# Optimization experiments

Measured on AMD Instinct MI355X. Metric: run time of the kernel, lower is better.

The kernel has to match this reference:

```python
import jax, jax.numpy as jnp
import numpy as np

B, N, C_Q, H, C_HID = 1, 2048, 256, 8, 32


def setup_inputs() -> dict:
    key = jax.random.key(0)
    ks = jax.random.split(key, 8)
    s_in = 1.0 / np.sqrt(C_Q)
    s_hid = 1.0 / np.sqrt(H * C_HID)
    return {
        "q_x": jax.random.normal(ks[0], (B, N, C_Q), jnp.float32),
        "kv_x": jax.random.normal(ks[1], (B, N, C_Q), jnp.float32),
        "attn_bias": jax.random.normal(ks[2], (B, H, N, N), jnp.float32),
        "Wq": jax.random.normal(ks[3], (C_Q, H * C_HID), jnp.float32) * s_in,
        "Wk": jax.random.normal(ks[4], (C_Q, H * C_HID), jnp.float32) * s_in,
        "Wv": jax.random.normal(ks[5], (C_Q, H * C_HID), jnp.float32) * s_in,
        "Wg": jax.random.normal(ks[6], (C_Q, H * C_HID), jnp.float32) * s_in,
        "Wo": jax.random.normal(ks[7], (H * C_HID, C_Q), jnp.float32) * s_hid,
    }


def reference(q_x, kv_x, attn_bias, Wq, Wk, Wv, Wg, Wo):
    # QKV projections (no bias), split heads: [B, H, N, C_hid]
    def proj(x, W):
        y = x @ W  # [B, N, H*C_hid]
        return y.reshape(y.shape[:-1] + (H, C_HID)).swapaxes(-2, -3)

    scale = 1.0 / np.sqrt(C_HID)
    q = proj(q_x, Wq) * scale
    k = proj(kv_x, Wk)
    v = proj(kv_x, Wv)

    # scores + external additive bias, stable softmax
    scores = jnp.einsum("bhqc,bhkc->bhqk", q, k) + attn_bias
    a = jax.nn.softmax(scores, axis=-1)
    o = jnp.einsum("bhqk,bhkc->bhqc", a, v)  # [B, H, N, C_hid]

    o = o.swapaxes(-2, -3)  # [B, N, H, C_hid]
    # sigmoid gating from query input
    g = jax.nn.sigmoid(q_x @ Wg).reshape(o.shape)
    o = o * g
    o = o.reshape(o.shape[:-2] + (H * C_HID,))
    return o @ Wo  # [B, N, C_q]
```

## Files before the change

kernel.cpp:

```cpp
#include <hip/hip_runtime.h>
#include <hip/hip_bf16.h>
#include <stdint.h>

typedef __attribute__((ext_vector_type(8))) short short8;
typedef __attribute__((ext_vector_type(8))) __bf16 bf16x8;
typedef __attribute__((ext_vector_type(4))) float f32x4;
typedef __attribute__((ext_vector_type(4))) float float4v;
typedef __attribute__((ext_vector_type(4))) unsigned short us4;
typedef unsigned int u32;
typedef __attribute__((ext_vector_type(2))) u32 u32x2;
typedef __attribute__((address_space(3))) u32 lds_u32;
typedef const __attribute__((address_space(1))) u32 g_u32;

#define NSEQ 2048
#define L2E 1.44269504088896f

static __device__ __forceinline__ unsigned short f2bf(float x){
  union { float f; u32 u; } v; v.f = x;
  u32 r = v.u + 0x7fffu + ((v.u >> 16) & 1u);
  return (unsigned short)(r >> 16);
}
static __device__ __forceinline__ float bf2f(unsigned short s){
  union { float f; u32 u; } v; v.u = ((u32)s) << 16; return v.f;
}
static __device__ __forceinline__ u32 cvtpk(float lo, float hi){
  u32 r; asm("v_cvt_pk_bf16_f32 %0, %1, %2" : "=v"(r) : "v"(lo), "v"(hi)); return r;
}
static __device__ __forceinline__ void gload16(const void* g, void* l){
  __builtin_amdgcn_global_load_lds((g_u32*)g, (lds_u32*)l, 16, 0, 0);
}
static __device__ __forceinline__ f32x4 mfma16(bf16x8 a, bf16x8 b, f32x4 c){
  return __builtin_amdgcn_mfma_f32_16x16x32_bf16(a, b, c, 0, 0, 0);
}
static __device__ __forceinline__ bf16x8 ldfrag(const void* p){
  return *(const bf16x8*)p;
}
#define MEMFENCE() asm volatile("" ::: "memory")

__global__ __launch_bounds__(256) void cvt_kernel(const float* __restrict__ qx,
                           const float* __restrict__ kvx,
                           const float* __restrict__ Wq, const float* __restrict__ Wk,
                           const float* __restrict__ Wv, const float* __restrict__ Wg,
                           const float* __restrict__ Wo,
                           unsigned short* __restrict__ Xbq, unsigned short* __restrict__ Xbkv,
                           unsigned short* __restrict__ Wt4, unsigned short* __restrict__ Wot){
  __shared__ float T[64][65];
  int bid = blockIdx.x;
  if (bid < 512){
    int i4 = (bid*256 + threadIdx.x) * 4;
    float4v q = *(const float4v*)(qx + i4);
    float4v k = *(const float4v*)(kvx + i4);
    us4 qo, ko;
    #pragma unroll
    for (int j = 0; j < 4; ++j){ qo[j] = f2bf(q[j]); ko[j] = f2bf(k[j]); }
    *(us4*)(Xbq + i4) = qo;
    *(us4*)(Xbkv + i4) = ko;
  } else {
    int b2 = bid - 512;
    int w = b2 >> 4, tile = b2 & 15, tr = tile >> 2, tc = tile & 3;
    const float* W = (w==0)?Wq:((w==1)?Wk:((w==2)?Wv:((w==3)?Wg:Wo)));
    int t = threadIdx.x;
    int rl = t >> 4, cq = t & 15;
    #pragma unroll
    for (int p = 0; p < 4; ++p){
      int r = p*16 + rl;
      float4v v = *(const float4v*)(W + (size_t)(tr*64 + r)*256 + tc*64 + cq*4);
      #pragma unroll
      for (int j = 0; j < 4; ++j) T[r][cq*4+j] = v[j];
    }
    __syncthreads();
    float s = (w==0) ? 0.17677669529663687f : 1.f;
    #pragma unroll
    for (int p = 0; p < 4; ++p){
      int o = p*16 + rl;
      us4 pk;
      #pragma unroll
      for (int j = 0; j < 4; ++j) pk[j] = f2bf(T[cq*4+j][o] * s);
      int og = tc*64 + o, ig = tr*64 + cq*4;
      if (w < 4) *(us4*)(Wt4 + (size_t)w*65536 + og*256 + ig) = pk;
      else       *(us4*)(Wot + (size_t)og*256 + ig) = pk;
    }
  }
}

__global__ __launch_bounds__(256) void proj_kernel(const unsigned short* __restrict__ Xbq,
     const unsigned short* __restrict__ Xbkv, const unsigned short* __restrict__ Wt4,
     unsigned short* __restrict__ Qb, unsigned short* __restrict__ Kb,
     unsigned short* __restrict__ Vt, unsigned short* __restrict__ Gg){
  __shared__ unsigned short Asm[64*256];
  __shared__ unsigned short Bsm[64*256];
  int mt = blockIdx.x;
  int nt = blockIdx.y;
  int col0 = nt * 64;
  int w = col0 >> 8;
  const unsigned short* A = (w==0 || w==3) ? Xbq : Xbkv;
  int tid = threadIdx.x, lane = tid & 63, wid = tid >> 6;
  const char* Ab = (const char*)A   + (size_t)mt*64*512;
  const char* Bb = (const char*)Wt4 + (size_t)col0*512;
  char* Asl = (char*)Asm; char* Bsl = (char*)Bsm;
  #pragma unroll
  for (int it = 0; it < 8; ++it){
    int o = it*4096 + wid*1024 + lane*16;
    int row = o >> 9, b = o & 511;
    int sb = (o & ~511) + (b ^ ((row & 15) << 4));
    gload16(Ab + sb, Asl + it*4096 + wid*1024);
    gload16(Bb + sb, Bsl + it*4096 + wid*1024);
  }
  __syncthreads();
  int ml = lane & 15, kg = lane >> 4;
  int m = wid*16 + ml;
  bf16x8 afr[8];
  #pragma unroll
  for (int ks = 0; ks < 8; ++ks)
    afr[ks] = ldfrag(Asl + m*512 + ((ks*64 + kg*16) ^ (ml << 4)));
  f32x4 acc[4];
  #pragma unroll
  for (int ct = 0; ct < 4; ++ct){
    acc[ct] = (f32x4){0.f,0.f,0.f,0.f};
    int oo = ct*16 + ml;
    #pragma unroll
    for (int ks = 0; ks < 8; ++ks){
      bf16x8 bfr = ldfrag(Bsl + oo*512 + ((ks*64 + kg*16) ^ (ml << 4)));
      acc[ct] = mfma16(afr[ks], bfr, acc[ct]);
    }
  }
  #pragma unroll
  for (int ct = 0; ct < 4; ++ct){
    int colg = col0 + ct*16 + ml;
    int cw = colg & 255, hh = cw >> 5, c = cw & 31;
    int n0 = mt*64 + wid*16 + kg*4;
    if (w == 2){
      us4 pk;
      pk[0]=f2bf(acc[ct][0]); pk[1]=f2bf(acc[ct][1]);
      pk[2]=f2bf(acc[ct][2]); pk[3]=f2bf(acc[ct][3]);
      *(us4*)((char*)Vt + ((size_t)(hh*32 + c)*NSEQ + n0)*2) = pk;
    } else {
      #pragma unroll
      for (int r = 0; r < 4; ++r){
        int n = n0 + r;
        float v = acc[ct][r];
        if (w == 0)      Qb[((size_t)hh*NSEQ + n)*32 + c] = f2bf(v);
        else if (w == 1) Kb[((size_t)hh*NSEQ + n)*32 + c] = f2bf(v);
        else             Gg[(size_t)n*256 + cw] = f2bf(1.f/(1.f + __expf(-v)));
      }
    }
  }
}

__global__ __launch_bounds__(256) void attn_kernel(const unsigned short* __restrict__ Qb,
    const unsigned short* __restrict__ Kb, const unsigned short* __restrict__ Vt,
    const float* __restrict__ bias,
    float* __restrict__ Opart, float* __restrict__ Mpart, float* __restrict__ Lpart){
  __shared__ unsigned short Ksm[4][2048];
  __shared__ unsigned short Vsm[4][2048];
  __shared__ unsigned short Psm[4096];
  int bid = blockIdx.x;
  int h = bid >> 7, qt = (bid >> 2) & 31, ch = bid & 3;
  int q0 = qt * 64;
  int tid = threadIdx.x, lane = tid & 63, wid = tid >> 6;
  int ml = lane & 15, kg = lane >> 4;
  int qw = q0 + wid*16;
  bf16x8 qfr = ldfrag((const char*)Qb + (((size_t)h*NSEQ + qw + ml)*32 + kg*8)*2);
  const char* Kbase = (const char*)Kb + (size_t)h*NSEQ*32*2;
  const char* Vbase = (const char*)Vt + (size_t)h*32*NSEQ*2;
  const float* bias_q = bias + (size_t)h*NSEQ*NSEQ + (size_t)(qw + ml)*NSEQ + ch*512 + kg*4;
  float mreg = -3e38f;
  float lreg = 0.f;
  f32x4 oacc[2];
  oacc[0] = (f32x4){0.f,0.f,0.f,0.f};
  oacc[1] = (f32x4){0.f,0.f,0.f,0.f};

  auto stage = [&](int t, int buf){
    int tg = ch*8 + t;
    int o = tid*16;
    int n = o >> 6, kb = o & 63;
    gload16(Kbase + (size_t)tg*4096 + (o & ~63) + (kb ^ (((n>>1)&3) << 4)),
            (char*)&Ksm[buf][0] + o);
    int c = o >> 7, vb = o & 127;
    gload16(Vbase + (size_t)c*4096 + (size_t)tg*128 + (vb ^ ((c&7) << 4)),
            (char*)&Vsm[buf][0] + o);
  };

  float4v bb[4];
  #pragma unroll
  for (int ct = 0; ct < 4; ++ct) bb[ct] = *(const float4v*)(bias_q + ct*16);
  MEMFENCE();
  stage(0, 0);
  stage(1, 1);
  int qrow = wid*16 + ml;
  char* Pb = (char*)Psm + qrow*128;
  int qs = (ml & 7) << 4;
  for (int t = 0; t < 8; ++t){
    int cur = t & 3;
    if (t == 7) asm volatile("s_waitcnt vmcnt(0)" ::: "memory");
    else        asm volatile("s_waitcnt vmcnt(2)" ::: "memory");
    __builtin_amdgcn_s_barrier();
    MEMFENCE();
    f32x4 s[4];
    #pragma unroll
    for (int ct = 0; ct < 4; ++ct){
      int n = ct*16 + ml;
      bf16x8 kfr = ldfrag((char*)&Ksm[cur][0] + n*64 + ((kg*16) ^ (((n>>1)&3) << 4)));
      f32x4 b;
      #pragma unroll
      for (int r = 0; r < 4; ++r) b[r] = bb[ct][r];
      s[ct] = mfma16(kfr, qfr, b);
    }
    MEMFENCE();
    if (t < 7){
      #pragma unroll
      for (int ct = 0; ct < 4; ++ct)
        bb[ct] = *(const float4v*)(bias_q + (t+1)*64 + ct*16);
    }
    MEMFENCE();
    if (t < 6) stage(t+2, (t+2) & 3);
    MEMFENCE();
    float m0 = fmaxf(fmaxf(s[0][0],s[0][1]), fmaxf(s[0][2],s[0][3]));
    float m1 = fmaxf(fmaxf(s[1][0],s[1][1]), fmaxf(s[1][2],s[1][3]));
    float m2 = fmaxf(fmaxf(s[2][0],s[2][1]), fmaxf(s[2][2],s[2][3]));
    float m3 = fmaxf(fmaxf(s[3][0],s[3][1]), fmaxf(s[3][2],s[3][3]));
    float mx = fmaxf(fmaxf(m0,m1), fmaxf(m2,m3));
    mx = fmaxf(mx, __shfl_xor(mx, 16));
    mx = fmaxf(mx, __shfl_xor(mx, 32));
    float mn = fmaxf(mreg, mx);
    float sc = exp2f((mreg - mn) * L2E);
    mreg = mn;
    float rs = 0.f;
    #pragma unroll
    for (int ct = 0; ct < 4; ++ct){
      #pragma unroll
      for (int r = 0; r < 4; ++r){
        float pv = exp2f((s[ct][r] - mn) * L2E);
        s[ct][r] = pv;
        rs += pv;
      }
    }
    rs += __shfl_xor(rs, 16);
    rs += __shfl_xor(rs, 32);
    lreg = lreg*sc + rs;
    float scq[4];
    #pragma unroll
    for (int r = 0; r < 4; ++r) scq[r] = __shfl(sc, kg*4 + r);
    #pragma unroll
    for (int c2 = 0; c2 < 2; ++c2){
      #pragma unroll
      for (int r = 0; r < 4; ++r) oacc[c2][r] *= scq[r];
    }
    #pragma unroll
    for (int ct = 0; ct < 4; ++ct){
      u32x2 pk;
      pk[0] = cvtpk(s[ct][0], s[ct][1]);
      pk[1] = cvtpk(s[ct][2], s[ct][3]);
      *(u32x2*)(Pb + ((ct*32 + kg*8) ^ qs)) = pk;
    }
    #pragma unroll
    for (int ks = 0; ks < 2; ++ks){
      bf16x8 pfr = ldfrag(Pb + ((ks*64 + kg*16) ^ qs));
      #pragma unroll
      for (int c2 = 0; c2 < 2; ++c2){
        int c = c2*16 + ml;
        bf16x8 vfr = ldfrag((char*)&Vsm[cur][0] + c*128 + ((ks*64 + kg*16) ^ ((c&7) << 4)));
        oacc[c2] = mfma16(pfr, vfr, oacc[c2]);
      }
    }
    MEMFENCE();
  }
  size_t pbase = ((size_t)(ch*8 + h)*NSEQ);
  if (kg == 0){
    Mpart[pbase + qw + ml] = mreg;
    Lpart[pbase + qw + ml] = lreg;
  }
  #pragma unroll
  for (int c2 = 0; c2 < 2; ++c2){
    #pragma unroll
    for (int r = 0; r < 4; ++r){
      int q = qw + kg*4 + r;
      Opart[(pbase + q)*32 + c2*16 + ml] = oacc[c2][r];
    }
  }
}

__global__ __launch_bounds__(256) void combine_kernel(const float* __restrict__ Opart,
    const float* __restrict__ Mpart, const float* __restrict__ Lpart,
    const unsigned short* __restrict__ Gg, unsigned short* __restrict__ Og){
  int n = blockIdx.x*8 + (threadIdx.x >> 5);
  int c = threadIdx.x & 31;
  #pragma unroll
  for (int h = 0; h < 8; ++h){
    float m0 = Mpart[(size_t)(0*8+h)*NSEQ + n], m1 = Mpart[(size_t)(1*8+h)*NSEQ + n];
    float m2 = Mpart[(size_t)(2*8+h)*NSEQ + n], m3 = Mpart[(size_t)(3*8+h)*NSEQ + n];
    float M = fmaxf(fmaxf(m0, m1), fmaxf(m2, m3));
    float e0 = exp2f((m0-M)*L2E), e1 = exp2f((m1-M)*L2E);
    float e2 = exp2f((m2-M)*L2E), e3 = exp2f((m3-M)*L2E);
    float L = Lpart[(size_t)(0*8+h)*NSEQ + n]*e0 + Lpart[(size_t)(1*8+h)*NSEQ + n]*e1
            + Lpart[(size_t)(2*8+h)*NSEQ + n]*e2 + Lpart[(size_t)(3*8+h)*NSEQ + n]*e3;
    float o = Opart[((size_t)(0*8+h)*NSEQ + n)*32 + c]*e0
            + Opart[((size_t)(1*8+h)*NSEQ + n)*32 + c]*e1
            + Opart[((size_t)(2*8+h)*NSEQ + n)*32 + c]*e2
            + Opart[((size_t)(3*8+h)*NSEQ + n)*32 + c]*e3;
    float g = bf2f(Gg[(size_t)n*256 + h*32 + c]);
    Og[(size_t)n*256 + h*32 + c] = f2bf(o / L * g);
  }
}

__global__ __launch_bounds__(256) void oproj_kernel(const unsigned short* __restrict__ Og,
    const unsigned short* __restrict__ Wot, float* __restrict__ out){
  __shared__ unsigned short Asm[64*256];
  __shared__ unsigned short Bsm[64*256];
  int mt = blockIdx.x, nt = blockIdx.y;
  int col0 = nt * 64;
  int tid = threadIdx.x, lane = tid & 63, wid = tid >> 6;
  const char* Ab = (const char*)Og  + (size_t)mt*64*512;
  const char* Bb = (const char*)Wot + (size_t)col0*512;
  char* Asl = (char*)Asm; char* Bsl = (char*)Bsm;
  #pragma unroll
  for (int it = 0; it < 8; ++it){
    int o = it*4096 + wid*1024 + lane*16;
    int row = o >> 9, b = o & 511;
    int sb = (o & ~511) + (b ^ ((row & 15) << 4));
    gload16(Ab + sb, Asl + it*4096 + wid*1024);
    gload16(Bb + sb, Bsl + it*4096 + wid*1024);
  }
  __syncthreads();
  int ml = lane & 15, kg = lane >> 4;
  int m = wid*16 + ml;
  bf16x8 afr[8];
  #pragma unroll
  for (int ks = 0; ks < 8; ++ks)
    afr[ks] = ldfrag(Asl + m*512 + ((ks*64 + kg*16) ^ (ml << 4)));
  f32x4 acc[4];
  #pragma unroll
  for (int ct = 0; ct < 4; ++ct){
    acc[ct] = (f32x4){0.f,0.f,0.f,0.f};
    int oo = ct*16 + ml;
    #pragma unroll
    for (int ks = 0; ks < 8; ++ks){
      bf16x8 bfr = ldfrag(Bsl + oo*512 + ((ks*64 + kg*16) ^ (ml << 4)));
      acc[ct] = mfma16(afr[ks], bfr, acc[ct]);
    }
  }
  #pragma unroll
  for (int ct = 0; ct < 4; ++ct){
    #pragma unroll
    for (int r = 0; r < 4; ++r){
      int mm = mt*64 + wid*16 + kg*4 + r;
      out[(size_t)mm*256 + col0 + ct*16 + ml] = acc[ct][r];
    }
  }
}

extern "C" void kernel_launch(void* const* d_in, const int* in_sizes, int n_in,
                              void* d_out, int out_size, void* d_ws, size_t ws_size,
                              hipStream_t stream) {
  const float* qx   = (const float*)d_in[0];
  const float* kvx  = (const float*)d_in[1];
  const float* bias = (const float*)d_in[2];
  const float* Wq   = (const float*)d_in[3];
  const float* Wk   = (const float*)d_in[4];
  const float* Wv   = (const float*)d_in[5];
  const float* Wg   = (const float*)d_in[6];
  const float* Wo   = (const float*)d_in[7];
  float* out = (float*)d_out;
  char* ws = (char*)d_ws;
  unsigned short* Xbq  = (unsigned short*)(ws);
  unsigned short* Xbkv = (unsigned short*)(ws + (1<<20));
  unsigned short* Wt4  = (unsigned short*)(ws + (2<<20));
  unsigned short* Wot  = (unsigned short*)(ws + (2<<20) + (512<<10));
  unsigned short* Qb   = (unsigned short*)(ws + (3<<20));
  unsigned short* Kb   = (unsigned short*)(ws + (4<<20));
  unsigned short* Vt   = (unsigned short*)(ws + (5<<20));
  unsigned short* Gg   = (unsigned short*)(ws + (6<<20));
  unsigned short* Og   = (unsigned short*)(ws + (7<<20));
  float*          Opart= (float*)(ws + (8<<20));
  float*          Mpart= (float*)(ws + (16<<20));
  float*          Lpart= (float*)(ws + (17<<20));

  cvt_kernel<<<592, 256, 0, stream>>>(qx, kvx, Wq, Wk, Wv, Wg, Wo, Xbq, Xbkv, Wt4, Wot);
  dim3 gp(32, 16);
  proj_kernel<<<gp, 256, 0, stream>>>(Xbq, Xbkv, Wt4, Qb, Kb, Vt, Gg);
  attn_kernel<<<1024, 256, 0, stream>>>(Qb, Kb, Vt, bias, Opart, Mpart, Lpart);
  combine_kernel<<<256, 256, 0, stream>>>(Opart, Mpart, Lpart, Gg, Og);
  dim3 go(32, 4);
  oproj_kernel<<<go, 256, 0, stream>>>(Og, Wot, out);
}
```

Measured before the change: 50.82 us.

## Load K/V MFMA fragments directly into registers, drop LDS staging and barriers

Replaces the LDS-staged, 4-buffer K/V pipeline with per-wave direct global loads of MFMA fragments into double-buffered registers, prefetched one tile ahead. This removes the block-wide barriers, vmcnt waits and LDS traffic for K and V. In exchange, all four waves each read the same K/V tiles from global/L2, with 16-byte loads strided across rows, and register pressure rises from the 16 extra fragment registers. The loop is also fully unrolled.

```diff
diff --git a/kernel.cpp b/kernel.cpp
--- a/kernel.cpp
+++ b/kernel.cpp
@@ -151,8 +151,6 @@
     const unsigned short* __restrict__ Kb, const unsigned short* __restrict__ Vt,
     const float* __restrict__ bias,
     float* __restrict__ Opart, float* __restrict__ Mpart, float* __restrict__ Lpart){
-  __shared__ unsigned short Ksm[4][2048];
-  __shared__ unsigned short Vsm[4][2048];
   __shared__ unsigned short Psm[4096];
   int bid = blockIdx.x;
   int h = bid >> 7, qt = (bid >> 2) & 31, ch = bid & 3;
@@ -161,8 +159,10 @@
   int ml = lane & 15, kg = lane >> 4;
   int qw = q0 + wid*16;
   bf16x8 qfr = ldfrag((const char*)Qb + (((size_t)h*NSEQ + qw + ml)*32 + kg*8)*2);
-  const char* Kbase = (const char*)Kb + (size_t)h*NSEQ*32*2;
-  const char* Vbase = (const char*)Vt + (size_t)h*32*NSEQ*2;
+  const char* Kl = (const char*)Kb + (size_t)h*NSEQ*64 + (size_t)ch*8*4096
+                   + ml*64 + kg*16;
+  const char* Vl = (const char*)Vt + (size_t)h*32*4096 + (size_t)ch*8*128
+                   + (size_t)ml*4096 + kg*16;
   const float* bias_q = bias + (size_t)h*NSEQ*NSEQ + (size_t)(qw + ml)*NSEQ + ch*512 + kg*4;
   float mreg = -3e38f;
   float lreg = 0.f;
@@ -170,51 +170,36 @@
   oacc[0] = (f32x4){0.f,0.f,0.f,0.f};
   oacc[1] = (f32x4){0.f,0.f,0.f,0.f};
 
-  auto stage = [&](int t, int buf){
-    int tg = ch*8 + t;
-    int o = tid*16;
-    int n = o >> 6, kb = o & 63;
-    gload16(Kbase + (size_t)tg*4096 + (o & ~63) + (kb ^ (((n>>1)&3) << 4)),
-            (char*)&Ksm[buf][0] + o);
-    int c = o >> 7, vb = o & 127;
-    gload16(Vbase + (size_t)c*4096 + (size_t)tg*128 + (vb ^ ((c&7) << 4)),
-            (char*)&Vsm[buf][0] + o);
-  };
-
   float4v bb[4];
+  bf16x8 kf[2][4];
+  bf16x8 vf[2][4];
   #pragma unroll
   for (int ct = 0; ct < 4; ++ct) bb[ct] = *(const float4v*)(bias_q + ct*16);
-  MEMFENCE();
-  stage(0, 0);
-  stage(1, 1);
+  #pragma unroll
+  for (int ct = 0; ct < 4; ++ct) kf[0][ct] = ldfrag(Kl + ct*1024);
+  #pragma unroll
+  for (int i = 0; i < 4; ++i) vf[0][i] = ldfrag(Vl + (size_t)(i&1)*65536 + (i>>1)*64);
   int qrow = wid*16 + ml;
   char* Pb = (char*)Psm + qrow*128;
   int qs = (ml & 7) << 4;
+  #pragma unroll
   for (int t = 0; t < 8; ++t){
-    int cur = t & 3;
-    if (t == 7) asm volatile("s_waitcnt vmcnt(0)" ::: "memory");
-    else        asm volatile("s_waitcnt vmcnt(2)" ::: "memory");
-    __builtin_amdgcn_s_barrier();
-    MEMFENCE();
+    int cur = t & 1, nxt = cur ^ 1;
     f32x4 s[4];
     #pragma unroll
-    for (int ct = 0; ct < 4; ++ct){
-      int n = ct*16 + ml;
-      bf16x8 kfr = ldfrag((char*)&Ksm[cur][0] + n*64 + ((kg*16) ^ (((n>>1)&3) << 4)));
-      f32x4 b;
-      #pragma unroll
-      for (int r = 0; r < 4; ++r) b[r] = bb[ct][r];
-      s[ct] = mfma16(kfr, qfr, b);
-    }
-    MEMFENCE();
+    for (int ct = 0; ct < 4; ++ct)
+      s[ct] = mfma16(kf[cur][ct], qfr, bb[ct]);
     if (t < 7){
       #pragma unroll
       for (int ct = 0; ct < 4; ++ct)
         bb[ct] = *(const float4v*)(bias_q + (t+1)*64 + ct*16);
-    }
-    MEMFENCE();
-    if (t < 6) stage(t+2, (t+2) & 3);
-    MEMFENCE();
+      #pragma unroll
+      for (int ct = 0; ct < 4; ++ct)
+        kf[nxt][ct] = ldfrag(Kl + (t+1)*4096 + ct*1024);
+      #pragma unroll
+      for (int i = 0; i < 4; ++i)
+        vf[nxt][i] = ldfrag(Vl + (size_t)(i&1)*65536 + (t+1)*128 + (i>>1)*64);
+    }
     float m0 = fmaxf(fmaxf(s[0][0],s[0][1]), fmaxf(s[0][2],s[0][3]));
     float m1 = fmaxf(fmaxf(s[1][0],s[1][1]), fmaxf(s[1][2],s[1][3]));
     float m2 = fmaxf(fmaxf(s[2][0],s[2][1]), fmaxf(s[2][2],s[2][3]));
@@ -257,11 +242,8 @@
     for (int ks = 0; ks < 2; ++ks){
       bf16x8 pfr = ldfrag(Pb + ((ks*64 + kg*16) ^ qs));
       #pragma unroll
-      for (int c2 = 0; c2 < 2; ++c2){
-        int c = c2*16 + ml;
-        bf16x8 vfr = ldfrag((char*)&Vsm[cur][0] + c*128 + ((ks*64 + kg*16) ^ ((c&7) << 4)));
-        oacc[c2] = mfma16(pfr, vfr, oacc[c2]);
-      }
+      for (int c2 = 0; c2 < 2; ++c2)
+        oacc[c2] = mfma16(pfr, vf[cur][ks*2+c2], oacc[c2]);
     }
     MEMFENCE();
   }
```

After: 64.11 us. 1.26x slower.
